# Optimization experiments

Measured on AMD Instinct MI355X. Metric: run time of the kernel, lower is better.

Reference implementation:

```python
import jax, jax.numpy as jnp
import numpy as np

B, T, D = 2, 2048, 2048
N, K, H = 16, 8, 128            # heads, kv heads, head_dim
SOFT_CAP = 50.0
WINDOW = 1024
SCALE = H ** -0.5               # query_pre_attn_scalar
ROPE_BASE = 10000.0
ROPE_SCALE = 1.0
K_MASK = -2.3819763e+38


def rms_norm(x, scale, eps=1e-6):
    var = jnp.mean(jnp.square(x), axis=-1, keepdims=True)
    return x * jax.lax.rsqrt(var + eps) * (1.0 + scale)


def apply_rope(x, positions):
    # x: [B,T,heads,H]; positions: [B,T] int
    head_dim = x.shape[-1]
    fraction = 2.0 * jnp.arange(head_dim // 2, dtype=jnp.float32) / head_dim
    timescale = ROPE_BASE ** fraction                      # [H/2]
    sinusoid = positions[..., None].astype(jnp.float32) / timescale  # [B,T,H/2]
    sinusoid = sinusoid[..., None, :] / ROPE_SCALE          # [B,T,1,H/2]
    sin, cos = jnp.sin(sinusoid), jnp.cos(sinusoid)
    first, second = jnp.split(x, 2, axis=-1)
    return jnp.concatenate([first * cos - second * sin,
                            second * cos + first * sin], axis=-1)


def setup_inputs() -> dict:
    key = jax.random.key(0)
    ks = jax.random.split(key, 6)
    x = jax.random.normal(ks[0], (B, T, D), jnp.float32)
    q_w = jax.random.normal(ks[1], (N, D, H), jnp.float32) * (D ** -0.5)
    kv_w = jax.random.normal(ks[2], (2, K, D, H), jnp.float32) * (D ** -0.5)
    o_w = jax.random.normal(ks[3], (N, H, D), jnp.float32) * ((N * H) ** -0.5)
    qnorm_scale = 0.1 * jax.random.normal(ks[4], (H,), jnp.float32)
    knorm_scale = 0.1 * jax.random.normal(ks[5], (H,), jnp.float32)
    segment_pos = jnp.broadcast_to(jnp.arange(T, dtype=jnp.int32), (B, T))
    attn_mask = jnp.broadcast_to(jnp.tril(jnp.ones((T, T), dtype=bool)), (B, T, T))
    return {"x": x, "q_w": q_w, "kv_w": kv_w, "o_w": o_w,
            "qnorm_scale": qnorm_scale, "knorm_scale": knorm_scale,
            "segment_pos": segment_pos, "attn_mask": attn_mask}


def reference(x, q_w, kv_w, o_w, qnorm_scale, knorm_scale, segment_pos, attn_mask):
    # projections
    q = jnp.einsum('BTD,NDH->BTNH', x, q_w)            # [B,T,N,H]
    k = jnp.einsum('BSD,KDH->BSKH', x, kv_w[0])        # [B,T,K,H]
    v = jnp.einsum('BSD,KDH->BSKH', x, kv_w[1])
    # QK RMSNorm, then RoPE, then query scaling (matches source order)
    q = apply_rope(rms_norm(q, qnorm_scale), segment_pos) * SCALE
    k = apply_rope(rms_norm(k, knorm_scale), segment_pos)
    # GQA: regroup query heads per kv head
    G = N // K
    qg = q.reshape(B, T, K, G, H)
    logits = jnp.einsum('BTKGH,BSKH->BTKGS', qg, k).reshape(B, T, N, T)
    # logit soft cap
    logits = jnp.tanh(logits / SOFT_CAP) * SOFT_CAP
    # sliding window mask combined with causal attn_mask
    pos_q = segment_pos[:, :, None]
    pos_k = segment_pos[:, None, :]
    sliding = (pos_k > pos_q - WINDOW) & (pos_k < pos_q + WINDOW)
    mask = attn_mask & sliding                          # [B,T,S]
    padded = jnp.where(mask[:, :, None, :], logits, K_MASK)
    probs = jax.nn.softmax(padded, axis=-1).astype(k.dtype)
    enc = jnp.einsum('BTKGS,BSKH->BTKGH',
                     probs.reshape(B, T, K, G, T), v).reshape(B, T, N, H)
    return jnp.einsum('BTNH,NHD->BTD', enc, o_w)
```

## Files before the change

kernel.cpp:

```cpp
#include <hip/hip_runtime.h>
#include <stdint.h>

#define BB 2
#define TT 2048
#define DD 2048
#define NHD 16
#define KVH 8
#define HD 128
#define JC 4096
#define WIN 1024
#define SCALE_Q 0.08838834764831845f

typedef __attribute__((ext_vector_type(8))) short bf16x8;
typedef __attribute__((ext_vector_type(8))) unsigned short us8;
typedef __attribute__((ext_vector_type(4))) unsigned short us4;
typedef __attribute__((ext_vector_type(4))) float f32x4;
typedef __attribute__((ext_vector_type(16))) float f32x16;
typedef __attribute__((ext_vector_type(4))) unsigned int u32x4;

#define GAS __attribute__((address_space(1)))
#define LAS __attribute__((address_space(3)))

__device__ __forceinline__ unsigned short f2bf(float f) {
  unsigned u = __float_as_uint(f);
  u += 0x7FFFu + ((u >> 16) & 1u);
  return (unsigned short)(u >> 16);
}

__device__ __forceinline__ void gload16(const void* g, void* l) {
  __builtin_amdgcn_global_load_lds((const GAS unsigned int*)g, (LAS unsigned int*)l, 16, 0, 0);
}

__global__ void __launch_bounds__(256) k_cvt(const float4* __restrict__ in,
                                             us4* __restrict__ out, int n4) {
  int i = blockIdx.x * 256 + threadIdx.x;
  if (i >= n4) return;
  float4 v = in[i];
  us4 o;
  o[0] = f2bf(v.x); o[1] = f2bf(v.y); o[2] = f2bf(v.z); o[3] = f2bf(v.w);
  out[i] = o;
}

__global__ void __launch_bounds__(256) k_transpose_cvt(
    const float* __restrict__ in, unsigned short* __restrict__ out,
    int R, int C, int ldin, long b0s, int nbi, long b1s, long obs) {
  __shared__ float tile[32][33];
  int z = blockIdx.z;
  const float* ib = in + (long)(z / nbi) * b0s + (long)(z % nbi) * b1s;
  unsigned short* ob = out + (long)z * obs;
  int c0 = blockIdx.x * 32, r0 = blockIdx.y * 32;
  int tx = threadIdx.x, ty = threadIdx.y;
#pragma unroll
  for (int i = 0; i < 4; i++)
    tile[ty + i * 8][tx] = ib[(long)(r0 + ty + i * 8) * ldin + c0 + tx];
  __syncthreads();
#pragma unroll
  for (int i = 0; i < 4; i++)
    ob[(long)(c0 + ty + i * 8) * R + r0 + tx] = f2bf(tile[tx][ty + i * 8]);
}

__global__ void __launch_bounds__(256, 2) k_gemm_bt(
    const unsigned short* __restrict__ A, const unsigned short* __restrict__ Bt,
    float* __restrict__ C, int M, int Nn, int Kd) {
  __shared__ short As[128 * 32];
  __shared__ short Bs[128 * 32];
  int tid = threadIdx.x;
  int lane = tid & 63, wid = tid >> 6;
  int wr = wid >> 1, wc = wid & 1;
  int m0 = blockIdx.x * 128, n0 = blockIdx.y * 128;
  f32x4 acc[4][4] = {};

  for (int ko = 0; ko < Kd; ko += 32) {
#pragma unroll
    for (int c = 0; c < 2; ++c) {
      int ch = wid * 2 + c;
      int row = ch * 16 + (lane >> 2);
      int col = (lane & 3) * 8;
      gload16(A + (long)(m0 + row) * Kd + ko + col, &As[ch * 512]);
      gload16(Bt + (long)(n0 + row) * Kd + ko + col, &Bs[ch * 512]);
    }
    __syncthreads();
    bf16x8 af[4], bf[4];
#pragma unroll
    for (int mi = 0; mi < 4; mi++)
      af[mi] = *(const bf16x8*)&As[(wr * 64 + mi * 16 + (lane & 15)) * 32 + (lane >> 4) * 8];
#pragma unroll
    for (int ni = 0; ni < 4; ni++)
      bf[ni] = *(const bf16x8*)&Bs[(wc * 64 + ni * 16 + (lane & 15)) * 32 + (lane >> 4) * 8];
#pragma unroll
    for (int mi = 0; mi < 4; mi++)
#pragma unroll
      for (int ni = 0; ni < 4; ni++)
        acc[mi][ni] = __builtin_amdgcn_mfma_f32_16x16x32_bf16(af[mi], bf[ni], acc[mi][ni], 0, 0, 0);
    __syncthreads();
  }
#pragma unroll
  for (int mi = 0; mi < 4; mi++)
#pragma unroll
    for (int ni = 0; ni < 4; ni++)
#pragma unroll
      for (int r = 0; r < 4; r++) {
        int row = m0 + wr * 64 + mi * 16 + (lane >> 4) * 4 + r;
        int col = n0 + wc * 64 + ni * 16 + (lane & 15);
        C[(long)row * Nn + col] = acc[mi][ni][r];
      }
}

__global__ void __launch_bounds__(256) k_norm_rope(
    const float* __restrict__ qkv, const float* __restrict__ qns, const float* __restrict__ kns,
    unsigned short* __restrict__ qb, unsigned short* __restrict__ kb) {
  int wid = threadIdx.x >> 6, lane = threadIdx.x & 63;
  long r = (long)blockIdx.x * 4 + wid;
  int b = (int)(r / (TT * 24));
  int rem = (int)(r % (TT * 24));
  int t = rem / 24, hd = rem % 24;
  const float* row = qkv + (long)(b * TT + t) * JC + (hd < 16 ? hd * HD : 2048 + (hd - 16) * HD);
  float f0 = row[lane], f1 = row[lane + 64];
  float ss = f0 * f0 + f1 * f1;
#pragma unroll
  for (int m = 1; m < 64; m <<= 1) ss += __shfl_xor(ss, m, 64);
  float rinv = rsqrtf(ss * (1.0f / 128.0f) + 1e-6f);
  const float* sc = (hd < 16) ? qns : kns;
  float y0 = f0 * rinv * (1.0f + sc[lane]);
  float y1 = f1 * rinv * (1.0f + sc[lane + 64]);
  float ts = exp2f((float)lane * (13.287712379549449f / 64.0f));
  float ang = (float)t / ts;
  float s, c;
  sincosf(ang, &s, &c);
  float o0 = y0 * c - y1 * s;
  float o1 = y1 * c + y0 * s;
  unsigned short* dst;
  if (hd < 16) {
    o0 *= SCALE_Q; o1 *= SCALE_Q;
    dst = qb + ((long)(b * NHD + hd) * TT + t) * HD;
  } else {
    dst = kb + ((long)(b * KVH + (hd - 16)) * TT + t) * HD;
  }
  dst[lane] = f2bf(o0);
  dst[lane + 64] = f2bf(o1);
}

template <bool FULL>
__device__ __forceinline__ void softcap16(const f32x16& s16, float* pr, float& lsum,
                                          int s_base, int tq, int g) {
#pragma unroll
  for (int r = 0; r < 16; r++) {
    float x = s16[r];
    float e = __builtin_amdgcn_exp2f(-0.05770780163555853f * fabsf(x));
    float u = (x > 0.0f ? e : 1.0f) * __builtin_amdgcn_rcpf(1.0f + e);
    float p = __builtin_amdgcn_exp2f(-144.26950408889634f * u);
    if (!FULL) {
      int s = s_base + (r & 3) + 8 * (r >> 2) + 4 * g;
      bool valid = (s <= tq) && (s > tq - WIN);
      p = valid ? p : 0.0f;
    }
    lsum += p;
    pr[r] = p;
  }
}

__device__ __forceinline__ void hswap(unsigned& a, unsigned& b, int g) {
  unsigned ax = (unsigned)__shfl_xor((int)a, 32, 64);
  unsigned bx = (unsigned)__shfl_xor((int)b, 32, 64);
  unsigned r0 = g ? bx : a;
  unsigned r1 = g ? b : ax;
  a = r0; b = r1;
}

__global__ void __launch_bounds__(256, 2) k_attn(
    const unsigned short* __restrict__ qb, const unsigned short* __restrict__ kb,
    const unsigned short* __restrict__ vbT, unsigned short* __restrict__ enc) {
  __shared__ short Kl[2][64][128];
  __shared__ short Vt[2][128][64];
  int tid = threadIdx.x, lane = tid & 63, w = tid >> 6;
  int g = lane >> 5, l31 = lane & 31;
  int id = blockIdx.x;
  int b = id >> 8;
  int rem = id & 255;
  int n = rem >> 4;
  int traw = rem & 15;
  int tile = b ? ((traw + 8) & 15) : traw;
  int t0 = tile * 128;
  int kh = n >> 1;
  const unsigned short* qbase = qb + ((long)(b * NHD + n) * TT + t0 + w * 32) * HD;
  const unsigned short* kbase = kb + (long)(b * KVH + kh) * TT * HD;
  const unsigned short* vbase = vbT + (long)(b * KVH + kh) * HD * TT;

  bf16x8 bq[8];
  {
    const unsigned short* qp = qbase + (long)l31 * HD + g * 8;
#pragma unroll
    for (int kb8 = 0; kb8 < 8; kb8++)
      bq[kb8] = *(const bf16x8*)(qp + kb8 * 16);
  }

  f32x16 acc[4] = {};
  float lsum = 0.0f;
  int t0w = t0 + w * 32;
  int tq = t0w + l31;
  int s_begin = (t0 >= WIN) ? t0 - WIN : 0;
  int s_end = t0 + 128;

  auto STAGE = [&](int buf, int s0) {
#pragma unroll
    for (int i = 0; i < 4; i++) {
      int row = w * 16 + i * 4 + (lane >> 4);
      int c16 = (lane & 15) ^ (row & 7);
      gload16(kbase + (long)(s0 + row) * HD + c16 * 8, &Kl[buf][w * 16 + i * 4][0]);
    }
#pragma unroll
    for (int i = 0; i < 4; i++) {
      int row = w * 32 + i * 8 + (lane >> 3);
      int c16 = (lane & 7) ^ (row & 7);
      gload16(vbase + (long)row * TT + s0 + c16 * 8, &Vt[buf][w * 32 + i * 8][0]);
    }
  };

  STAGE(0, s_begin);
  __syncthreads();
  int cur = 0;
  for (int s0 = s_begin; s0 < s_end; s0 += 64) {
    if (s0 + 64 < s_end) STAGE(cur ^ 1, s0 + 64);
    bool live = (s0 <= t0w + 31) && (s0 + 63 >= t0w - (WIN - 1));
    if (live) {
      f32x16 sc2[2] = {};
#pragma unroll
      for (int sb = 0; sb < 2; sb++) {
        int srow = sb * 32 + l31;
#pragma unroll
        for (int kb8 = 0; kb8 < 8; kb8++) {
          bf16x8 ak = *(const bf16x8*)&Kl[cur][srow][8 * ((2 * kb8 + g) ^ (srow & 7))];
          sc2[sb] = __builtin_amdgcn_mfma_f32_32x32x16_bf16(ak, bq[kb8], sc2[sb], 0, 0, 0);
        }
      }
      bool full = (s0 + 63 <= t0w) && (s0 >= t0w + 31 - (WIN - 1));
      unsigned pw[4][4];
#pragma unroll
      for (int sb = 0; sb < 2; sb++) {
        float pr[16];
        if (full) softcap16<true>(sc2[sb], pr, lsum, 0, tq, g);
        else      softcap16<false>(sc2[sb], pr, lsum, s0 + sb * 32, tq, g);
        unsigned X[4], Y[4];
#pragma unroll
        for (int m = 0; m < 4; m++) {
          asm("v_cvt_pk_bf16_f32 %0, %1, %2" : "=v"(X[m]) : "v"(pr[4 * m]), "v"(pr[4 * m + 1]));
          asm("v_cvt_pk_bf16_f32 %0, %1, %2" : "=v"(Y[m]) : "v"(pr[4 * m + 2]), "v"(pr[4 * m + 3]));
        }
#pragma unroll
        for (int kl = 0; kl < 2; kl++) {
          hswap(X[2 * kl], X[2 * kl + 1], g);
          hswap(Y[2 * kl], Y[2 * kl + 1], g);
          pw[sb * 2 + kl][0] = X[2 * kl];
          pw[sb * 2 + kl][1] = Y[2 * kl];
          pw[sb * 2 + kl][2] = X[2 * kl + 1];
          pw[sb * 2 + kl][3] = Y[2 * kl + 1];
        }
      }
#pragma unroll
      for (int ks = 0; ks < 4; ks++) {
        u32x4 t4 = {pw[ks][0], pw[ks][1], pw[ks][2], pw[ks][3]};
        bf16x8 pb = __builtin_bit_cast(bf16x8, t4);
#pragma unroll
        for (int ht = 0; ht < 4; ht++) {
          int hrow = ht * 32 + l31;
          bf16x8 av = *(const bf16x8*)&Vt[cur][hrow][8 * ((2 * ks + g) ^ (hrow & 7))];
          acc[ht] = __builtin_amdgcn_mfma_f32_32x32x16_bf16(av, pb, acc[ht], 0, 0, 0);
        }
      }
    }
    __syncthreads();
    cur ^= 1;
  }

  lsum += __shfl_xor(lsum, 32, 64);
  float inv = __builtin_amdgcn_rcpf(lsum);
  unsigned short* dst = enc + ((long)(b * TT + tq) * NHD + n) * HD;
#pragma unroll
  for (int ht = 0; ht < 4; ht++)
#pragma unroll
    for (int r4 = 0; r4 < 4; r4++) {
      us4 o;
#pragma unroll
      for (int e = 0; e < 4; e++) o[e] = f2bf(acc[ht][r4 * 4 + e] * inv);
      *(us4*)(dst + ht * 32 + 8 * r4 + 4 * g) = o;
    }
}

extern "C" void kernel_launch(void* const* d_in, const int* in_sizes, int n_in,
                              void* d_out, int out_size, void* d_ws, size_t ws_size,
                              hipStream_t stream) {
  const float* x    = (const float*)d_in[0];
  const float* q_w  = (const float*)d_in[1];
  const float* kv_w = (const float*)d_in[2];
  const float* o_w  = (const float*)d_in[3];
  const float* qns  = (const float*)d_in[4];
  const float* kns  = (const float*)d_in[5];

  if (ws_size < (104ull << 20)) return;
  char* ws = (char*)d_ws;
  float*          qkv  = (float*)(ws + 0);
  unsigned short* enc  = (unsigned short*)(ws + 0);
  unsigned short* x_bf = (unsigned short*)(ws + (64ll << 20));
  unsigned short* qb   = (unsigned short*)(ws + (64ll << 20));
  unsigned short* Wt   = (unsigned short*)(ws + (80ll << 20));
  unsigned short* kb   = (unsigned short*)(ws + (80ll << 20));
  unsigned short* vbT  = (unsigned short*)(ws + (88ll << 20));
  unsigned short* Wt_o = (unsigned short*)(ws + (96ll << 20));

  dim3 tb(32, 8, 1);
  k_cvt<<<8192, 256, 0, stream>>>((const float4*)x, (us4*)x_bf, 2097152);
  k_transpose_cvt<<<dim3(4, 64, 16), tb, 0, stream>>>(q_w, Wt, 2048, 128, 128,
                                                      0, 16, (long)2048 * 128, (long)128 * 2048);
  k_transpose_cvt<<<dim3(4, 64, 8), tb, 0, stream>>>(kv_w, Wt + (long)2048 * 2048, 2048, 128, 128,
                                                     0, 8, (long)2048 * 128, (long)128 * 2048);
  k_transpose_cvt<<<dim3(4, 64, 8), tb, 0, stream>>>(kv_w + (long)8 * 2048 * 128, Wt + (long)3072 * 2048,
                                                     2048, 128, 128, 0, 8, (long)2048 * 128, (long)128 * 2048);
  k_transpose_cvt<<<dim3(64, 64, 1), tb, 0, stream>>>(o_w, Wt_o, 2048, 2048, 2048, 0, 1, 0, 0);
  k_gemm_bt<<<dim3(32, 32), 256, 0, stream>>>(x_bf, Wt, qkv, 4096, 4096, 2048);
  k_transpose_cvt<<<dim3(4, 64, 16), tb, 0, stream>>>(qkv + 3072, vbT, 2048, 128, 4096,
                                                      (long)2048 * 4096, 8, 128, (long)128 * 2048);
  k_norm_rope<<<24576, 256, 0, stream>>>(qkv, qns, kns, qb, kb);
  k_attn<<<512, 256, 0, stream>>>(qb, kb, vbT, enc);
  k_gemm_bt<<<dim3(32, 16), 256, 0, stream>>>(enc, Wt_o, (float*)d_out, 4096, 2048, 2048);
}
```

Baseline: 243.4 us.

## Replace projection GEMMs with 8-wave triple-buffered swizzled-LDS GEMM

Replaces the simple 128x128, single-buffered GEMM with a 256x128-tile, 512-thread kernel that triple-buffers K=64 slices in LDS. Loads are issued two iterations ahead and paced with vmcnt waits. It also XOR-swizzles the LDS layout to avoid bank conflicts, remaps block IDs across XCDs for L2 locality, and raises wave priority around the MFMA bursts. The goal is to hide global-load latency and remove the per-iteration barrier stalls of the old kernel, at the cost of much more LDS (about 147KB per block) and more complex synchronisation.

```diff
diff --git a/kernel.cpp b/kernel.cpp
--- a/kernel.cpp
+++ b/kernel.cpp
@@ -59,49 +59,92 @@
     ob[(long)(c0 + ty + i * 8) * R + r0 + tx] = f2bf(tile[tx][ty + i * 8]);
 }
 
-__global__ void __launch_bounds__(256, 2) k_gemm_bt(
+__global__ void __launch_bounds__(512, 2) k_gemm8(
     const unsigned short* __restrict__ A, const unsigned short* __restrict__ Bt,
-    float* __restrict__ C, int M, int Nn, int Kd) {
-  __shared__ short As[128 * 32];
-  __shared__ short Bs[128 * 32];
-  int tid = threadIdx.x;
-  int lane = tid & 63, wid = tid >> 6;
-  int wr = wid >> 1, wc = wid & 1;
-  int m0 = blockIdx.x * 128, n0 = blockIdx.y * 128;
+    float* __restrict__ C, int M, int Nn, int Kd, int nby) {
+  __shared__ short lds[3][384 * 64];
+  int tid = threadIdx.x, lane = tid & 63, w = tid >> 6;
+  int wm = w >> 1, wn = w & 1;
+  int id = blockIdx.x;
+  int cpx = gridDim.x >> 3;
+  id = (id & 7) * cpx + (id >> 3);
+  int m0 = (id / nby) * 256, n0 = (id % nby) * 128;
+  const int NT = Kd >> 6;
+
+  auto STG = [&](int sb, int ko, int j0, int j1) {
+#pragma unroll
+    for (int j = j0; j <= j1; ++j) {
+      int cdata = (lane & 7) ^ (lane >> 3);
+      if (j < 4) {
+        int rbase = j * 64 + w * 8;
+        int row = rbase + (lane >> 3);
+        gload16(A + (long)(m0 + row) * Kd + ko + cdata * 8, &lds[sb][rbase * 64]);
+      } else {
+        int rbase = (j - 4) * 64 + w * 8;
+        int row = rbase + (lane >> 3);
+        gload16(Bt + (long)(n0 + row) * Kd + ko + cdata * 8, &lds[sb][(256 + rbase) * 64]);
+      }
+    }
+  };
+
   f32x4 acc[4][4] = {};
-
-  for (int ko = 0; ko < Kd; ko += 32) {
-#pragma unroll
-    for (int c = 0; c < 2; ++c) {
-      int ch = wid * 2 + c;
-      int row = ch * 16 + (lane >> 2);
-      int col = (lane & 3) * 8;
-      gload16(A + (long)(m0 + row) * Kd + ko + col, &As[ch * 512]);
-      gload16(Bt + (long)(n0 + row) * Kd + ko + col, &Bs[ch * 512]);
-    }
-    __syncthreads();
-    bf16x8 af[4], bf[4];
-#pragma unroll
-    for (int mi = 0; mi < 4; mi++)
-      af[mi] = *(const bf16x8*)&As[(wr * 64 + mi * 16 + (lane & 15)) * 32 + (lane >> 4) * 8];
+  STG(0, 0, 0, 5);
+  STG(1, 64, 0, 5);
+  asm volatile("s_waitcnt vmcnt(6)" ::: "memory");
+  __builtin_amdgcn_s_barrier();
+
+  int buf = 0, sbuf = 2;
+  for (int t = 0; t < NT; ++t) {
+    bool st = (t + 2) < NT;
+#pragma unroll
+    for (int q = 0; q < 2; ++q) {
+      bf16x8 af[2][2], bfr[4][2];
+#pragma unroll
+      for (int mi2 = 0; mi2 < 2; mi2++)
+#pragma unroll
+        for (int kk = 0; kk < 2; kk++) {
+          int row = wm * 64 + (q * 2 + mi2) * 16 + (lane & 15);
+          int c = ((kk << 2) + (lane >> 4)) ^ (row & 7);
+          af[mi2][kk] = *(const bf16x8*)&lds[buf][row * 64 + c * 8];
+        }
+#pragma unroll
+      for (int ni = 0; ni < 4; ni++)
+#pragma unroll
+        for (int kk = 0; kk < 2; kk++) {
+          int row = wn * 64 + ni * 16 + (lane & 15);
+          int c = ((kk << 2) + (lane >> 4)) ^ (row & 7);
+          bfr[ni][kk] = *(const bf16x8*)&lds[buf][(256 + row) * 64 + c * 8];
+        }
+      if (st) STG(sbuf, (t + 2) << 6, q * 3, q * 3 + 2);
+      if (q == 1) {
+        if (st) asm volatile("s_waitcnt vmcnt(6)" ::: "memory");
+        else    asm volatile("s_waitcnt vmcnt(0)" ::: "memory");
+      }
+      __builtin_amdgcn_s_barrier();
+      __builtin_amdgcn_s_setprio(1);
+#pragma unroll
+      for (int mi2 = 0; mi2 < 2; mi2++)
+#pragma unroll
+        for (int ni = 0; ni < 4; ni++)
+#pragma unroll
+          for (int kk = 0; kk < 2; kk++)
+            acc[q * 2 + mi2][ni] = __builtin_amdgcn_mfma_f32_16x16x32_bf16(
+                af[mi2][kk], bfr[ni][kk], acc[q * 2 + mi2][ni], 0, 0, 0);
+      __builtin_amdgcn_s_setprio(0);
+      __builtin_amdgcn_s_barrier();
+    }
+    buf = (buf == 2) ? 0 : buf + 1;
+    sbuf = (sbuf == 2) ? 0 : sbuf + 1;
+  }
+
+#pragma unroll
+  for (int mi = 0; mi < 4; mi++)
 #pragma unroll
     for (int ni = 0; ni < 4; ni++)
-      bf[ni] = *(const bf16x8*)&Bs[(wc * 64 + ni * 16 + (lane & 15)) * 32 + (lane >> 4) * 8];
-#pragma unroll
-    for (int mi = 0; mi < 4; mi++)
-#pragma unroll
-      for (int ni = 0; ni < 4; ni++)
-        acc[mi][ni] = __builtin_amdgcn_mfma_f32_16x16x32_bf16(af[mi], bf[ni], acc[mi][ni], 0, 0, 0);
-    __syncthreads();
-  }
-#pragma unroll
-  for (int mi = 0; mi < 4; mi++)
-#pragma unroll
-    for (int ni = 0; ni < 4; ni++)
 #pragma unroll
       for (int r = 0; r < 4; r++) {
-        int row = m0 + wr * 64 + mi * 16 + (lane >> 4) * 4 + r;
-        int col = n0 + wc * 64 + ni * 16 + (lane & 15);
+        int row = m0 + wm * 64 + mi * 16 + (lane >> 4) * 4 + r;
+        int col = n0 + wn * 64 + ni * 16 + (lane & 15);
         C[(long)row * Nn + col] = acc[mi][ni][r];
       }
 }
@@ -316,10 +359,10 @@
   k_transpose_cvt<<<dim3(4, 64, 8), tb, 0, stream>>>(kv_w + (long)8 * 2048 * 128, Wt + (long)3072 * 2048,
                                                      2048, 128, 128, 0, 8, (long)2048 * 128, (long)128 * 2048);
   k_transpose_cvt<<<dim3(64, 64, 1), tb, 0, stream>>>(o_w, Wt_o, 2048, 2048, 2048, 0, 1, 0, 0);
-  k_gemm_bt<<<dim3(32, 32), 256, 0, stream>>>(x_bf, Wt, qkv, 4096, 4096, 2048);
+  k_gemm8<<<512, 512, 0, stream>>>(x_bf, Wt, qkv, 4096, 4096, 2048, 32);
   k_transpose_cvt<<<dim3(4, 64, 16), tb, 0, stream>>>(qkv + 3072, vbT, 2048, 128, 4096,
                                                       (long)2048 * 4096, 8, 128, (long)128 * 2048);
   k_norm_rope<<<24576, 256, 0, stream>>>(qkv, qns, kns, qb, kb);
   k_attn<<<512, 256, 0, stream>>>(qb, kb, vbT, enc);
-  k_gemm_bt<<<dim3(32, 16), 256, 0, stream>>>(enc, Wt_o, (float*)d_out, 4096, 2048, 2048);
-}
+  k_gemm8<<<256, 512, 0, stream>>>(enc, Wt_o, (float*)d_out, 4096, 2048, 2048, 16);
+}
```

Measured after the change: 239.8 us. Within noise of the previous version (-1.5%).

## Replace GEMM with 4-stage pipelined, swizzled, larger-tile 512-thread kernel

Applied to the files above, without the earlier changes.

Replaces the simple single-buffered 128x128 GEMM with a templated kernel that uses 256x256 or 128x256 tiles, 8 waves, and a 4-deep LDS ring buffer with explicit vmcnt waits. Global loads are issued three stages ahead and interleaved with the MFMA halves. It adds an XOR swizzle against LDS bank conflicts, s_setprio around the MFMA blocks, and XCD-aware block remapping for L2 locality. The cost is more LDS and registers per block, hardcoded K=2048, and fragile hand-written wait counts.

```diff
diff --git a/kernel.cpp b/kernel.cpp
--- a/kernel.cpp
+++ b/kernel.cpp
@@ -59,49 +59,114 @@
     ob[(long)(c0 + ty + i * 8) * R + r0 + tx] = f2bf(tile[tx][ty + i * 8]);
 }
 
-__global__ void __launch_bounds__(256, 2) k_gemm_bt(
+template <int BM, int BN>
+__global__ void __launch_bounds__(512, 2) k_gemm9(
     const unsigned short* __restrict__ A, const unsigned short* __restrict__ Bt,
-    float* __restrict__ C, int M, int Nn, int Kd) {
-  __shared__ short As[128 * 32];
-  __shared__ short Bs[128 * 32];
-  int tid = threadIdx.x;
-  int lane = tid & 63, wid = tid >> 6;
-  int wr = wid >> 1, wc = wid & 1;
-  int m0 = blockIdx.x * 128, n0 = blockIdx.y * 128;
-  f32x4 acc[4][4] = {};
-
-  for (int ko = 0; ko < Kd; ko += 32) {
-#pragma unroll
-    for (int c = 0; c < 2; ++c) {
-      int ch = wid * 2 + c;
-      int row = ch * 16 + (lane >> 2);
-      int col = (lane & 3) * 8;
-      gload16(A + (long)(m0 + row) * Kd + ko + col, &As[ch * 512]);
-      gload16(Bt + (long)(n0 + row) * Kd + ko + col, &Bs[ch * 512]);
-    }
-    __syncthreads();
-    bf16x8 af[4], bf[4];
-#pragma unroll
-    for (int mi = 0; mi < 4; mi++)
-      af[mi] = *(const bf16x8*)&As[(wr * 64 + mi * 16 + (lane & 15)) * 32 + (lane >> 4) * 8];
+    float* __restrict__ C, int M, int Nn, int nby) {
+  constexpr int KD = 2048;
+  constexpr int NT = KD / 32;
+  constexpr int ROWS = BM + BN;
+  constexpr int IA = BM / 128;
+  constexpr int IPT = IA + BN / 128;
+  constexpr int MT = BM / 32;
+  constexpr int MT2 = MT / 2;
+  __shared__ short lds[4][ROWS * 32];
+
+  int tid = threadIdx.x, lane = tid & 63, w = tid >> 6;
+  int wm = w >> 2, wn = w & 3;
+  int id = blockIdx.x;
+  int cpx = gridDim.x >> 3;
+  id = (id & 7) * cpx + (id >> 3);
+  int m0 = (id / nby) * BM, n0 = (id % nby) * BN;
+
+  int srow = tid >> 2;
+  int scol = ((tid & 3) ^ (srow & 3)) * 8;
+  const unsigned short* gA = A + (long)(m0 + srow) * KD + scol;
+  const unsigned short* gB = Bt + (long)(n0 + srow) * KD + scol;
+
+  auto STG = [&](int p, int ko, int j) {
+    if (j < IA)
+      gload16(gA + (long)j * 128 * KD + ko, &lds[p][(j * 128 + w * 16) * 32]);
+    else
+      gload16(gB + (long)(j - IA) * 128 * KD + ko, &lds[p][(BM + (j - IA) * 128 + w * 16) * 32]);
+  };
+
+  int frag = (lane & 15) * 32 + (((lane >> 4) ^ (lane & 3)) * 8);
+  int abase = wm * (BM / 2) * 32 + frag;
+  int bbase = (BM + wn * 64) * 32 + frag;
+
+  f32x4 acc[MT][4] = {};
+#pragma unroll
+  for (int tt = 0; tt < 3; ++tt)
+#pragma unroll
+    for (int j = 0; j < IPT; ++j) STG(tt, tt * 32, j);
+  if constexpr (IPT == 4) asm volatile("s_waitcnt vmcnt(8)" ::: "memory");
+  else                    asm volatile("s_waitcnt vmcnt(6)" ::: "memory");
+  __builtin_amdgcn_s_barrier();
+
+  for (int t = 0; t < NT; ++t) {
+    const short* bufp = lds[t & 3];
+    bool st = (t + 3) < NT;
+    int ko = (t & 31) * 32 + 96;
+    ko = (t + 3) * 32;
+    int sp = (t + 3) & 3;
+    bf16x8 bfr[4], af[MT2];
+#pragma unroll
+    for (int ni = 0; ni < 4; ++ni)
+      bfr[ni] = *(const bf16x8*)&bufp[bbase + ni * 16 * 32];
+#pragma unroll
+    for (int mi = 0; mi < MT2; ++mi)
+      af[mi] = *(const bf16x8*)&bufp[abase + mi * 16 * 32];
+    if (st) { STG(sp, ko, 0); STG(sp, ko, 1); }
+    __builtin_amdgcn_s_barrier();
+    asm volatile("s_waitcnt lgkmcnt(0)" ::: "memory");
+    __builtin_amdgcn_sched_barrier(0);
+    __builtin_amdgcn_s_setprio(1);
+#pragma unroll
+    for (int mi = 0; mi < MT2; ++mi)
+#pragma unroll
+      for (int ni = 0; ni < 4; ++ni)
+        acc[mi][ni] = __builtin_amdgcn_mfma_f32_16x16x32_bf16(af[mi], bfr[ni], acc[mi][ni], 0, 0, 0);
+    __builtin_amdgcn_s_setprio(0);
+    __builtin_amdgcn_s_barrier();
+    bf16x8 af2[MT2];
+#pragma unroll
+    for (int mi = 0; mi < MT2; ++mi)
+      af2[mi] = *(const bf16x8*)&bufp[abase + (MT2 + mi) * 16 * 32];
+    if (st) {
+#pragma unroll
+      for (int j = 2; j < IPT; ++j) STG(sp, ko, j);
+    }
+    if constexpr (IPT == 4) {
+      if (t < NT - 3)       asm volatile("s_waitcnt vmcnt(8)" ::: "memory");
+      else if (t == NT - 3) asm volatile("s_waitcnt vmcnt(4)" ::: "memory");
+      else if (t < NT - 1)  asm volatile("s_waitcnt vmcnt(0)" ::: "memory");
+    } else {
+      if (t < NT - 3)       asm volatile("s_waitcnt vmcnt(6)" ::: "memory");
+      else if (t == NT - 3) asm volatile("s_waitcnt vmcnt(3)" ::: "memory");
+      else if (t < NT - 1)  asm volatile("s_waitcnt vmcnt(0)" ::: "memory");
+    }
+    __builtin_amdgcn_s_barrier();
+    asm volatile("s_waitcnt lgkmcnt(0)" ::: "memory");
+    __builtin_amdgcn_sched_barrier(0);
+    __builtin_amdgcn_s_setprio(1);
+#pragma unroll
+    for (int mi = 0; mi < MT2; ++mi)
+#pragma unroll
+      for (int ni = 0; ni < 4; ++ni)
+        acc[MT2 + mi][ni] = __builtin_amdgcn_mfma_f32_16x16x32_bf16(af2[mi], bfr[ni], acc[MT2 + mi][ni], 0, 0, 0);
+    __builtin_amdgcn_s_setprio(0);
+    __builtin_amdgcn_s_barrier();
+  }
+
+#pragma unroll
+  for (int mi = 0; mi < MT; mi++)
 #pragma unroll
     for (int ni = 0; ni < 4; ni++)
-      bf[ni] = *(const bf16x8*)&Bs[(wc * 64 + ni * 16 + (lane & 15)) * 32 + (lane >> 4) * 8];
-#pragma unroll
-    for (int mi = 0; mi < 4; mi++)
-#pragma unroll
-      for (int ni = 0; ni < 4; ni++)
-        acc[mi][ni] = __builtin_amdgcn_mfma_f32_16x16x32_bf16(af[mi], bf[ni], acc[mi][ni], 0, 0, 0);
-    __syncthreads();
-  }
-#pragma unroll
-  for (int mi = 0; mi < 4; mi++)
-#pragma unroll
-    for (int ni = 0; ni < 4; ni++)
 #pragma unroll
       for (int r = 0; r < 4; r++) {
-        int row = m0 + wr * 64 + mi * 16 + (lane >> 4) * 4 + r;
-        int col = n0 + wc * 64 + ni * 16 + (lane & 15);
+        int row = m0 + wm * (BM / 2) + mi * 16 + (lane >> 4) * 4 + r;
+        int col = n0 + wn * 64 + ni * 16 + (lane & 15);
         C[(long)row * Nn + col] = acc[mi][ni][r];
       }
 }
@@ -316,10 +381,10 @@
   k_transpose_cvt<<<dim3(4, 64, 8), tb, 0, stream>>>(kv_w + (long)8 * 2048 * 128, Wt + (long)3072 * 2048,
                                                      2048, 128, 128, 0, 8, (long)2048 * 128, (long)128 * 2048);
   k_transpose_cvt<<<dim3(64, 64, 1), tb, 0, stream>>>(o_w, Wt_o, 2048, 2048, 2048, 0, 1, 0, 0);
-  k_gemm_bt<<<dim3(32, 32), 256, 0, stream>>>(x_bf, Wt, qkv, 4096, 4096, 2048);
+  k_gemm9<256, 256><<<256, 512, 0, stream>>>(x_bf, Wt, qkv, 4096, 4096, 16);
   k_transpose_cvt<<<dim3(4, 64, 16), tb, 0, stream>>>(qkv + 3072, vbT, 2048, 128, 4096,
                                                       (long)2048 * 4096, 8, 128, (long)128 * 2048);
   k_norm_rope<<<24576, 256, 0, stream>>>(qkv, qns, kns, qb, kb);
   k_attn<<<512, 256, 0, stream>>>(qb, kb, vbT, enc);
-  k_gemm_bt<<<dim3(32, 16), 256, 0, stream>>>(enc, Wt_o, (float*)d_out, 4096, 2048, 2048);
-}
+  k_gemm9<128, 256><<<256, 512, 0, stream>>>(enc, Wt_o, (float*)d_out, 4096, 2048, 8);
+}
```

New measurement: 232.1 us. 4.7% less time.
